# Optimization experiments

Measured on AMD Instinct MI355X. Metric: run time of the kernel, lower is better.

## Reference

```python
import jax, jax.numpy as jnp
import numpy as np
import math

N_HEADS = 16
D_Q = 1024
D_K = 1024
D_V = 1024
D_OUT = 1024
HID = D_OUT // N_HEADS  # 64
BATCH = 2
SEQ = 2048


def setup_inputs() -> dict:
    key = jax.random.key(0)
    ks = jax.random.split(key, 7)
    stdv = 1.0 / math.sqrt(HID)
    so = 1.0 / math.sqrt(D_OUT)
    return {
        "q": jax.random.normal(ks[0], (BATCH, SEQ, D_Q), dtype=jnp.float32),
        "k": jax.random.normal(ks[1], (BATCH, SEQ, D_K), dtype=jnp.float32),
        "v": jax.random.normal(ks[2], (BATCH, SEQ, D_V), dtype=jnp.float32),
        "W_query": jax.random.uniform(ks[3], (N_HEADS, D_Q, HID), jnp.float32, -stdv, stdv),
        "W_key": jax.random.uniform(ks[4], (N_HEADS, D_K, HID), jnp.float32, -stdv, stdv),
        "W_val": jax.random.uniform(ks[5], (N_HEADS, D_V, HID), jnp.float32, -stdv, stdv),
        "W_out": jax.random.uniform(ks[6], (N_HEADS, HID, D_OUT), jnp.float32, -so, so),
    }


def reference(q, k, v, W_query, W_key, W_val, W_out):
    norm = 1.0 / math.sqrt(HID)
    # per-head projections: [h, b, s, e]
    Q = jnp.einsum("bqd,hde->hbqe", q, W_query)
    K = jnp.einsum("bkd,hde->hbke", k, W_key)
    V = jnp.einsum("bkd,hde->hbke", v, W_val)
    # scaled dot-product attention
    compat = norm * jnp.einsum("hbqe,hbke->hbqk", Q, K)
    attn = jax.nn.softmax(compat, axis=-1)
    heads = jnp.einsum("hbqk,hbke->hbqe", attn, V)
    # output projection: concat heads then W_out == sum over h of per-head proj
    out = jnp.einsum("hbqe,heo->bqo", heads, W_out)
    return out
```

## Files before the change

### kernel.cpp

```cpp
#include <hip/hip_runtime.h>
#include <hip/hip_bf16.h>

typedef __bf16 bf16;
typedef __bf16 bf16x8 __attribute__((ext_vector_type(8)));
typedef __bf16 bf16x4 __attribute__((ext_vector_type(4)));
typedef float  f32x4  __attribute__((ext_vector_type(4)));

#define MFMA16(a,b,c) __builtin_amdgcn_mfma_f32_16x16x32_bf16(a, b, c, 0, 0, 0)

__device__ __forceinline__ void gl2lds16(const bf16* g, bf16* l) {
    __builtin_amdgcn_global_load_lds(
        (__attribute__((address_space(1))) void*)g,
        (__attribute__((address_space(3))) void*)l, 16, 0, 0);
}

__global__ __launch_bounds__(256)
void prep_kernel(const float* __restrict__ q, const float* __restrict__ k,
                 const float* __restrict__ v, const float* __restrict__ Wq,
                 const float* __restrict__ Wk, const float* __restrict__ Wv,
                 const float* __restrict__ Wo, bf16* __restrict__ Xcat,
                 bf16* __restrict__ Wqkv, bf16* __restrict__ Wot)
{
    __shared__ bf16 Tl[64][72];
    const int bid = blockIdx.x;
    const int tid = threadIdx.x;

    if (bid < 6144) {
        int gidx = bid * 256 + tid;
        int t    = gidx >> 19;
        int off  = (gidx & 0x7FFFF) * 8;
        const float* src = (t == 0) ? q : (t == 1) ? k : v;
        const float4 f0 = *(const float4*)&src[off];
        const float4 f1 = *(const float4*)&src[off + 4];
        bf16x8 p = { (bf16)f0.x, (bf16)f0.y, (bf16)f0.z, (bf16)f0.w,
                     (bf16)f1.x, (bf16)f1.y, (bf16)f1.z, (bf16)f1.w };
        *(bf16x8*)&Xcat[(size_t)gidx * 8] = p;
        return;
    }
    if (bid < 6912) {
        int idx = bid - 6144;
        int x = idx & 15, z = idx >> 4;
        int t = z >> 4, h = z & 15;
        const float* inp = ((t == 0) ? Wq : (t == 1) ? Wk : Wv) + (size_t)h * 65536;
        bf16* outp = Wqkv + (size_t)t * 1024 * 1024 + (size_t)h * 65536;
        int r0 = x * 64;
        #pragma unroll
        for (int i = 0; i < 2; i++) {
            int s = tid + i * 256;
            int r = s >> 3, c8 = (s & 7) * 8;
            const float* ap = &inp[(size_t)(r0 + r) * 64 + c8];
            float4 f0 = *(const float4*)ap;
            float4 f1 = *(const float4*)(ap + 4);
            bf16x8 p = { (bf16)f0.x, (bf16)f0.y, (bf16)f0.z, (bf16)f0.w,
                         (bf16)f1.x, (bf16)f1.y, (bf16)f1.z, (bf16)f1.w };
            *(bf16x8*)&Tl[r][c8] = p;
        }
        __syncthreads();
        #pragma unroll
        for (int i = 0; i < 2; i++) {
            int s = tid + i * 256;
            int c = s >> 3, r8 = (s & 7) * 8;
            bf16x8 p;
            #pragma unroll
            for (int j = 0; j < 8; j++) p[j] = Tl[r8 + j][c];
            *(bf16x8*)&outp[(size_t)c * 1024 + r0 + r8] = p;
        }
        return;
    }
    {
        int idx = bid - 6912;
        int y = idx & 15, h = idx >> 4;
        int c0 = y * 64;
        const float* inp = Wo + (size_t)h * 65536;
        bf16* outp = Wot + (size_t)h * 64;
        #pragma unroll
        for (int i = 0; i < 2; i++) {
            int s = tid + i * 256;
            int r = s >> 3, c8 = (s & 7) * 8;
            const float* ap = &inp[(size_t)r * 1024 + c0 + c8];
            float4 f0 = *(const float4*)ap;
            float4 f1 = *(const float4*)(ap + 4);
            bf16x8 p = { (bf16)f0.x, (bf16)f0.y, (bf16)f0.z, (bf16)f0.w,
                         (bf16)f1.x, (bf16)f1.y, (bf16)f1.z, (bf16)f1.w };
            *(bf16x8*)&Tl[r][c8] = p;
        }
        __syncthreads();
        #pragma unroll
        for (int i = 0; i < 2; i++) {
            int s = tid + i * 256;
            int c = s >> 3, r8 = (s & 7) * 8;
            bf16x8 p;
            #pragma unroll
            for (int j = 0; j < 8; j++) p[j] = Tl[r8 + j][c];
            *(bf16x8*)&outp[(size_t)(c0 + c) * 1024 + r8] = p;
        }
    }
}

__global__ __launch_bounds__(256)
void qkv_gemm(const bf16* __restrict__ Xcat, const bf16* __restrict__ Wqkv,
              bf16* __restrict__ Cq, bf16* __restrict__ Ck, bf16* __restrict__ Vt,
              float qscale)
{
    __shared__ bf16 Al[2][128 * 64];
    __shared__ bf16 Bl[2][128 * 64];
    const int slab  = blockIdx.x >> 5;
    const int mbase = (blockIdx.x & 31) * 128;
    const int nbase = blockIdx.y * 128;
    const int tid = threadIdx.x;
    const int w = tid >> 6, lane = tid & 63;
    const int lm = lane & 15, q4 = lane >> 4;
    const int wr = (w >> 1) * 64, wc = (w & 1) * 64;
    const int lrow = lane >> 3, lsw = ((lane & 7) ^ lrow) * 8;

    const bf16* A  = Xcat + (size_t)slab * 4096 * 1024;
    const bf16* Bt = Wqkv + (size_t)slab * 1024 * 1024;

    f32x4 acc[4][4] = {};

    auto stage = [&](int k0, int d) {
        #pragma unroll
        for (int i = 0; i < 4; i++) {
            int c = w * 4 + i;
            gl2lds16(&A [(size_t)(mbase + c * 8 + lrow) * 1024 + k0 + lsw], &Al[d][c * 512]);
            gl2lds16(&Bt[(size_t)(nbase + c * 8 + lrow) * 1024 + k0 + lsw], &Bl[d][c * 512]);
        }
    };

    stage(0, 0);

    for (int t = 0; t < 16; t++) {
        __syncthreads();
        if (t < 15) stage((t + 1) * 64, (t + 1) & 1);
        const bf16* Ad = &Al[t & 1][0];
        const bf16* Bd = &Bl[t & 1][0];
        __builtin_amdgcn_s_setprio(1);
        #pragma unroll
        for (int kk2 = 0; kk2 < 2; kk2++) {
            bf16x8 a[4], bfr[4];
            const int g = ((kk2 * 4 + q4) ^ (lm & 7)) * 8;
            #pragma unroll
            for (int i = 0; i < 4; i++) a[i]   = *(const bf16x8*)&Ad[(wr + i * 16 + lm) * 64 + g];
            #pragma unroll
            for (int j = 0; j < 4; j++) bfr[j] = *(const bf16x8*)&Bd[(wc + j * 16 + lm) * 64 + g];
            #pragma unroll
            for (int i = 0; i < 4; i++)
                #pragma unroll
                for (int j = 0; j < 4; j++)
                    acc[i][j] = MFMA16(a[i], bfr[j], acc[i][j]);
        }
        __builtin_amdgcn_s_setprio(0);
    }

    if (slab == 2) {
        #pragma unroll
        for (int i = 0; i < 4; i++)
            #pragma unroll
            for (int j = 0; j < 4; j++) {
                int s0  = mbase + wr + i * 16 + q4 * 4;
                int col = nbase + wc + j * 16 + lm;
                int sp  = (s0 & ~31) | (((s0 >> 2) & 3) * 8) | (((s0 >> 4) & 1) * 4);
                bf16x4 p = { (bf16)acc[i][j][0], (bf16)acc[i][j][1],
                             (bf16)acc[i][j][2], (bf16)acc[i][j][3] };
                *(bf16x4*)&Vt[(size_t)col * 4096 + sp] = p;
            }
    } else {
        bf16* C = (slab == 0) ? Cq : Ck;
        const float scale = (slab == 0) ? qscale : 1.0f;
        #pragma unroll
        for (int i = 0; i < 4; i++)
            #pragma unroll
            for (int j = 0; j < 4; j++)
                #pragma unroll
                for (int r = 0; r < 4; r++) {
                    int row = mbase + wr + i * 16 + q4 * 4 + r;
                    int col = nbase + wc + j * 16 + lm;
                    C[(size_t)row * 1024 + col] = (bf16)(acc[i][j][r] * scale);
                }
    }
}

__global__ __launch_bounds__(256)
void outproj_gemm(const bf16* __restrict__ A, const bf16* __restrict__ Bt,
                  float* __restrict__ C)
{
    __shared__ bf16 Al[2][64 * 64];
    __shared__ bf16 Bl[2][128 * 64];
    const int mbase = blockIdx.x * 64;
    const int nbase = blockIdx.y * 128;
    const int tid = threadIdx.x;
    const int w = tid >> 6, lane = tid & 63;
    const int lm = lane & 15, q4 = lane >> 4;
    const int wm = (w >> 1) * 32, wn = (w & 1) * 64;
    const int lrow = lane >> 3, lsw = ((lane & 7) ^ lrow) * 8;

    f32x4 acc[2][4] = {};

    auto stage = [&](int k0, int d) {
        #pragma unroll
        for (int i = 0; i < 2; i++) {
            int c = w * 2 + i;
            gl2lds16(&A[(size_t)(mbase + c * 8 + lrow) * 1024 + k0 + lsw], &Al[d][c * 512]);
        }
        #pragma unroll
        for (int i = 0; i < 4; i++) {
            int c = w * 4 + i;
            gl2lds16(&Bt[(size_t)(nbase + c * 8 + lrow) * 1024 + k0 + lsw], &Bl[d][c * 512]);
        }
    };

    stage(0, 0);

    for (int t = 0; t < 16; t++) {
        __syncthreads();
        if (t < 15) stage((t + 1) * 64, (t + 1) & 1);
        const bf16* Ad = &Al[t & 1][0];
        const bf16* Bd = &Bl[t & 1][0];
        __builtin_amdgcn_s_setprio(1);
        #pragma unroll
        for (int kk2 = 0; kk2 < 2; kk2++) {
            bf16x8 a[2], bfr[4];
            const int g = ((kk2 * 4 + q4) ^ (lm & 7)) * 8;
            #pragma unroll
            for (int i = 0; i < 2; i++) a[i]   = *(const bf16x8*)&Ad[(wm + i * 16 + lm) * 64 + g];
            #pragma unroll
            for (int j = 0; j < 4; j++) bfr[j] = *(const bf16x8*)&Bd[(wn + j * 16 + lm) * 64 + g];
            #pragma unroll
            for (int i = 0; i < 2; i++)
                #pragma unroll
                for (int j = 0; j < 4; j++)
                    acc[i][j] = MFMA16(a[i], bfr[j], acc[i][j]);
        }
        __builtin_amdgcn_s_setprio(0);
    }

    #pragma unroll
    for (int i = 0; i < 2; i++)
        #pragma unroll
        for (int j = 0; j < 4; j++)
            #pragma unroll
            for (int r = 0; r < 4; r++) {
                int row = mbase + wm + i * 16 + q4 * 4 + r;
                int col = nbase + wn + j * 16 + lm;
                C[(size_t)row * 1024 + col] = acc[i][j][r];
            }
}

__global__ __launch_bounds__(256, 2)
void attn_kernel(const bf16* __restrict__ Qp, const bf16* __restrict__ Kp,
                 const bf16* __restrict__ Vt, bf16* __restrict__ Hd)
{
    __shared__ bf16 KV[4][64 * 64];
    __shared__ float Ls[128];

    const int n  = blockIdx.x + 16 * (blockIdx.y + 2 * blockIdx.z);
    const int m  = (n & 7) * 64 + (n >> 3);
    const int qt = m & 15, bh = m >> 4;
    const int b  = bh & 1,  h  = bh >> 1;

    const int qbase = qt * 128;
    const int tid  = threadIdx.x;
    const int w    = tid >> 6, lane = tid & 63;
    const int p    = w & 1;
    const int kvh  = w >> 1;
    const int lm   = lane & 15, q4 = lane >> 4;
    const int lrow = lane >> 3, lsw = ((lane & 7) ^ lrow) * 8;

    const bf16* Qh = Qp + (size_t)(b * 2048 + qbase + p * 64) * 1024 + h * 64;
    const bf16* Kh = Kp + (size_t)(b * 2048) * 1024 + h * 64;
    const bf16* Vh = Vt + (size_t)(h * 64) * 4096 + b * 2048;

    bf16x8 Qf[4][2];
    #pragma unroll
    for (int i = 0; i < 4; i++)
        #pragma unroll
        for (int kk2 = 0; kk2 < 2; kk2++)
            Qf[i][kk2] = *(const bf16x8*)&Qh[(size_t)(i * 16 + lm) * 1024 + kk2 * 32 + q4 * 8];

    const bf16 one = (bf16)1.0f;
    const bf16x8 ones = { one, one, one, one, one, one, one, one };

    f32x4 O[4][4] = {};
    f32x4 Lacc[4] = {};

    auto stage = [&](int kt, int d) {
        #pragma unroll
        for (int i = 0; i < 2; i++) {
            int c = w * 2 + i;
            gl2lds16(&Kh[(size_t)(kt * 64 + c * 8 + lrow) * 1024 + lsw], &KV[d][c * 512]);
            gl2lds16(&Vh[(size_t)(c * 8 + lrow) * 4096 + kt * 64 + lsw], &KV[2 + d][c * 512]);
        }
    };

    stage(0, 0);

    for (int it = 0; it < 32; it++) {
        __syncthreads();
        if (it < 31) stage(it + 1, (it + 1) & 1);
        const bf16* Kd = &KV[it & 1][0];
        const bf16* Vd = &KV[2 + (it & 1)][0];

        f32x4 St[4][2] = {};
        __builtin_amdgcn_s_setprio(1);
        #pragma unroll
        for (int c2 = 0; c2 < 2; c2++) {
            const int ctp = kvh * 2 + c2;
            #pragma unroll
            for (int kk2 = 0; kk2 < 2; kk2++) {
                const int g = ((kk2 * 4 + q4) ^ (lm & 7)) * 8;
                bf16x8 kf = *(const bf16x8*)&Kd[(ctp * 16 + lm) * 64 + g];
                #pragma unroll
                for (int i = 0; i < 4; i++)
                    St[i][c2] = MFMA16(kf, Qf[i][kk2], St[i][c2]);
            }
        }
        __builtin_amdgcn_s_setprio(0);

        bf16x8 Pf[4];
        #pragma unroll
        for (int i = 0; i < 4; i++)
            #pragma unroll
            for (int j = 0; j < 8; j++)
                Pf[i][j] = (bf16)__builtin_amdgcn_exp2f(St[i][j >> 2][j & 3]);

        __builtin_amdgcn_s_setprio(1);
        #pragma unroll
        for (int i = 0; i < 4; i++) Lacc[i] = MFMA16(Pf[i], ones, Lacc[i]);
        const int gv = ((kvh * 4 + q4) ^ (lm & 7)) * 8;
        #pragma unroll
        for (int et = 0; et < 4; et++) {
            bf16x8 vf = *(const bf16x8*)&Vd[(et * 16 + lm) * 64 + gv];
            #pragma unroll
            for (int i = 0; i < 4; i++)
                O[i][et] = MFMA16(Pf[i], vf, O[i][et]);
        }
        __builtin_amdgcn_s_setprio(0);
    }

    __syncthreads();
    float* Ol = (float*)&KV[0][0];
    if (kvh == 1) {
        #pragma unroll
        for (int i = 0; i < 4; i++)
            #pragma unroll
            for (int et = 0; et < 4; et++)
                #pragma unroll
                for (int r = 0; r < 4; r++)
                    Ol[(p * 64 + i * 16 + q4 * 4 + r) * 64 + et * 16 + lm] = O[i][et][r];
        if (lm == 0) {
            #pragma unroll
            for (int i = 0; i < 4; i++)
                #pragma unroll
                for (int r = 0; r < 4; r++)
                    Ls[p * 64 + i * 16 + q4 * 4 + r] = Lacc[i][r];
        }
    }
    __syncthreads();
    if (kvh == 0) {
        #pragma unroll
        for (int i = 0; i < 4; i++) {
            float rl[4];
            #pragma unroll
            for (int r = 0; r < 4; r++)
                rl[r] = 1.0f / (Lacc[i][r] + Ls[p * 64 + i * 16 + q4 * 4 + r]);
            #pragma unroll
            for (int et = 0; et < 4; et++)
                #pragma unroll
                for (int r = 0; r < 4; r++) {
                    float o = O[i][et][r] +
                              Ol[(p * 64 + i * 16 + q4 * 4 + r) * 64 + et * 16 + lm];
                    int row = b * 2048 + qbase + p * 64 + i * 16 + q4 * 4 + r;
                    Hd[(size_t)row * 1024 + h * 64 + et * 16 + lm] = (bf16)(o * rl[r]);
                }
        }
    }
}

extern "C" void kernel_launch(void* const* d_in, const int* in_sizes, int n_in,
                              void* d_out, int out_size, void* d_ws, size_t ws_size,
                              hipStream_t stream)
{
    const float* q  = (const float*)d_in[0];
    const float* k  = (const float*)d_in[1];
    const float* v  = (const float*)d_in[2];
    const float* Wq = (const float*)d_in[3];
    const float* Wk = (const float*)d_in[4];
    const float* Wv = (const float*)d_in[5];
    const float* Wo = (const float*)d_in[6];
    float* out = (float*)d_out;

    const size_t Mi = 1024 * 1024;
    bf16* Xcat  = (bf16*)d_ws;
    bf16* Hd    = Xcat;
    bf16* Wqkv  = Xcat + 12 * Mi;
    bf16* Wot   = Xcat + 15 * Mi;
    bf16* Qproj = Xcat + 16 * Mi;
    bf16* Kproj = Xcat + 20 * Mi;
    bf16* Vtb   = (bf16*)d_out;

    const float qscale = 0.125f * 1.4426950408889634f;

    prep_kernel<<<7168, 256, 0, stream>>>(q, k, v, Wq, Wk, Wv, Wo, Xcat, Wqkv, Wot);
    qkv_gemm<<<dim3(96, 8), 256, 0, stream>>>(Xcat, Wqkv, Qproj, Kproj, Vtb, qscale);
    attn_kernel<<<dim3(16, 2, 16), 256, 0, stream>>>(Qproj, Kproj, Vtb, Hd);
    outproj_gemm<<<dim3(64, 8), 256, 0, stream>>>(Hd, Wot, out);
}
```

Before: 202.2 us.

## Software-pipeline attention loop with triple-buffered K/V and overlapped S/PV

Restructures the attention inner loop into a software pipeline. K/V tiles are triple-buffered in LDS, and the QK^T score MFMAs for the next tile are issued alongside the exp and PV MFMAs of the current tile, using two ping-pong score register sets. The aim is more independent MFMA work per barrier, hiding exp and LDS latency. In exchange it uses more LDS (6 tiles instead of 4) and more registers, which may reduce occupancy under the 2-blocks-per-CU launch bound.

```diff
diff --git a/kernel.cpp b/kernel.cpp
--- a/kernel.cpp
+++ b/kernel.cpp
@@ -250,7 +250,7 @@
 void attn_kernel(const bf16* __restrict__ Qp, const bf16* __restrict__ Kp,
                  const bf16* __restrict__ Vt, bf16* __restrict__ Hd)
 {
-    __shared__ bf16 KV[4][64 * 64];
+    __shared__ bf16 KV[6][64 * 64];
     __shared__ float Ls[128];
 
     const int n  = blockIdx.x + 16 * (blockIdx.y + 2 * blockIdx.z);
@@ -282,26 +282,23 @@
 
     f32x4 O[4][4] = {};
     f32x4 Lacc[4] = {};
-
-    auto stage = [&](int kt, int d) {
+    f32x4 StA[4][2], StB[4][2];
+
+    auto stage = [&](int kt, bf16* kd, bf16* vd) {
         #pragma unroll
         for (int i = 0; i < 2; i++) {
             int c = w * 2 + i;
-            gl2lds16(&Kh[(size_t)(kt * 64 + c * 8 + lrow) * 1024 + lsw], &KV[d][c * 512]);
-            gl2lds16(&Vh[(size_t)(c * 8 + lrow) * 4096 + kt * 64 + lsw], &KV[2 + d][c * 512]);
+            gl2lds16(&Kh[(size_t)(kt * 64 + c * 8 + lrow) * 1024 + lsw], &kd[c * 512]);
+            gl2lds16(&Vh[(size_t)(c * 8 + lrow) * 4096 + kt * 64 + lsw], &vd[c * 512]);
         }
     };
 
-    stage(0, 0);
-
-    for (int it = 0; it < 32; it++) {
-        __syncthreads();
-        if (it < 31) stage(it + 1, (it + 1) & 1);
-        const bf16* Kd = &KV[it & 1][0];
-        const bf16* Vd = &KV[2 + (it & 1)][0];
-
-        f32x4 St[4][2] = {};
-        __builtin_amdgcn_s_setprio(1);
+    auto S_step = [&](const bf16* Kd, f32x4 (&St)[4][2]) {
+        #pragma unroll
+        for (int i = 0; i < 4; i++)
+            #pragma unroll
+            for (int c2 = 0; c2 < 2; c2++)
+                St[i][c2] = f32x4{0.f, 0.f, 0.f, 0.f};
         #pragma unroll
         for (int c2 = 0; c2 < 2; c2++) {
             const int ctp = kvh * 2 + c2;
@@ -314,16 +311,15 @@
                     St[i][c2] = MFMA16(kf, Qf[i][kk2], St[i][c2]);
             }
         }
-        __builtin_amdgcn_s_setprio(0);
-
+    };
+
+    auto PV_step = [&](const bf16* Vd, const f32x4 (&St)[4][2]) {
         bf16x8 Pf[4];
         #pragma unroll
         for (int i = 0; i < 4; i++)
             #pragma unroll
             for (int j = 0; j < 8; j++)
                 Pf[i][j] = (bf16)__builtin_amdgcn_exp2f(St[i][j >> 2][j & 3]);
-
-        __builtin_amdgcn_s_setprio(1);
         #pragma unroll
         for (int i = 0; i < 4; i++) Lacc[i] = MFMA16(Pf[i], ones, Lacc[i]);
         const int gv = ((kvh * 4 + q4) ^ (lm & 7)) * 8;
@@ -334,8 +330,43 @@
             for (int i = 0; i < 4; i++)
                 O[i][et] = MFMA16(Pf[i], vf, O[i][et]);
         }
+    };
+
+    bf16 *cK0 = &KV[0][0], *cK1 = &KV[1][0], *cK2 = &KV[2][0];
+    bf16 *cV0 = &KV[3][0], *cV1 = &KV[4][0], *cV2 = &KV[5][0];
+
+    stage(0, cK0, cV0);
+    stage(1, cK1, cV1);
+    __syncthreads();
+    S_step(cK0, StA);
+
+    #pragma unroll 1
+    for (int t2 = 0; t2 < 15; t2++) {
+        __syncthreads();
+        stage(2 * t2 + 2, cK2, cV2);
+        __builtin_amdgcn_s_setprio(1);
+        S_step(cK1, StB);
+        PV_step(cV0, StA);
         __builtin_amdgcn_s_setprio(0);
-    }
+        { bf16* t = cK0; cK0 = cK1; cK1 = cK2; cK2 = t;
+          t = cV0; cV0 = cV1; cV1 = cV2; cV2 = t; }
+        __syncthreads();
+        stage(2 * t2 + 3, cK2, cV2);
+        __builtin_amdgcn_s_setprio(1);
+        S_step(cK1, StA);
+        PV_step(cV0, StB);
+        __builtin_amdgcn_s_setprio(0);
+        { bf16* t = cK0; cK0 = cK1; cK1 = cK2; cK2 = t;
+          t = cV0; cV0 = cV1; cV1 = cV2; cV2 = t; }
+    }
+    __syncthreads();
+    __builtin_amdgcn_s_setprio(1);
+    S_step(cK1, StB);
+    PV_step(cV0, StA);
+    __builtin_amdgcn_s_setprio(0);
+    { bf16* t = cK0; cK0 = cK1; cK1 = cK2; cK2 = t;
+      t = cV0; cV0 = cV1; cV1 = cV2; cV2 = t; }
+    PV_step(cV0, StB);
 
     __syncthreads();
     float* Ol = (float*)&KV[0][0];
```

Result: no change. 198.6 us (-1.8%).
